# Kernel optimization log

Measured on AMD Instinct MI355X. Metric: run time of the kernel, lower is better.

## Reference

```python
import jax, jax.numpy as jnp
import numpy as np

B, N, H = 2048, 5, 5
IN, HID, OUT = 7, 2048, 512  # IN = 1 + c + c^2 with c = (H-1)//2 = 2


def setup_inputs() -> dict:
    key = jax.random.key(0)
    ks = jax.random.split(key, 7)
    k_in = 1.0 / np.sqrt(IN).astype(np.float32)
    k_h = 1.0 / np.sqrt(HID).astype(np.float32)
    return {
        "ins": jax.random.normal(ks[0], (B, N, H, H), jnp.float32),
        "w1": (jax.random.uniform(ks[1], (4, HID, IN), jnp.float32) - 0.5) * k_in,
        "b1": (jax.random.uniform(ks[2], (HID,), jnp.float32) - 0.5) * k_in,
        "w2": (jax.random.uniform(ks[3], (4, HID, HID), jnp.float32) - 0.5) * k_h,
        "b2": (jax.random.uniform(ks[4], (HID,), jnp.float32) - 0.5) * k_h,
        "w3": (jax.random.uniform(ks[5], (4, OUT, HID), jnp.float32) - 0.5) * k_h,
        "b3": (jax.random.uniform(ks[6], (OUT,), jnp.float32) - 0.5) * k_h,
        "ln_g": jnp.ones((HID,), jnp.float32),
        "ln_b": jnp.zeros((HID,), jnp.float32),
    }


def _rot90(x):
    # matches torch: x.flip(3).permute(0,1,3,2)
    return jnp.swapaxes(jnp.flip(x, axis=3), 2, 3)


def _orbit_stack(x):
    b, n = x.shape[0], x.shape[1]
    c = (x.shape[-1] - 1) // 2  # = 2 for H=5
    center = x[:, :, c, c]  # (B,N)
    parts = []
    xi = x
    for _ in range(4):  # fixed C4 group orbit, not a data loop
        parts.append(xi[:, :, :c, :c + 1].reshape(b, n, -1))  # (B,N,c+c^2)
        xi = _rot90(xi)
    orb = jnp.stack(parts, axis=-1)  # (B,N,c+c^2,4)
    cen = jnp.broadcast_to(center[..., None, None], (b, n, 1, 4))
    out = jnp.concatenate([cen, orb], axis=2)  # (B,N,n_orbits,4)
    return jnp.transpose(out, (0, 1, 3, 2))  # (B,N,4,n_orbits)


def _c4conv(w, bias, x):
    # block-circulant kernel: mat[g,h] = w[(h-g) % 4]
    mat = jnp.stack([jnp.roll(w, i, axis=0) for i in range(4)], axis=0)  # (4,4,out,in)
    return jnp.einsum('ghij,bnhj->bngi', mat, x) + bias


def _layernorm(x, g, b, eps=1e-5):
    m = jnp.mean(x, axis=-1, keepdims=True)
    v = jnp.mean(jnp.square(x - m), axis=-1, keepdims=True)
    return (x - m) / jnp.sqrt(v + eps) * g + b


def reference(ins, w1, b1, w2, b2, w3, b3, ln_g, ln_b):
    h = _orbit_stack(ins)                          # (B,N,4,7)
    h = jax.nn.relu(_c4conv(w1, b1, h))            # (B,N,4,HID)
    h = jax.nn.relu(_layernorm(_c4conv(w2, b2, h), ln_g, ln_b))
    return _c4conv(w3, b3, h)                      # (B,N,4,OUT)
```

## Files before the change

kernel.cpp:

```cpp
#include <hip/hip_runtime.h>
#include <stdint.h>


#define HID 2048
#define MROWS 10240

typedef float floatx4 __attribute__((ext_vector_type(4)));
typedef __bf16 bf16x8 __attribute__((ext_vector_type(8)));

__device__ __forceinline__ unsigned short f2bf(float f) {
  union { float f; unsigned int u; } v; v.f = f;
  unsigned int r = v.u + 0x7fffu + ((v.u >> 16) & 1u);
  return (unsigned short)(r >> 16);
}
__device__ __forceinline__ float bf2f(unsigned short s) {
  union { unsigned int u; float f; } v; v.u = ((unsigned int)s) << 16;
  return v.f;
}

template <int NO>
__global__ __launch_bounds__(256) void wtrans_kernel(const float* __restrict__ w,
                                                     unsigned short* __restrict__ W0s,
                                                     unsigned short* __restrict__ W2s,
                                                     unsigned short* __restrict__ Bc) {
  int idx = blockIdx.x * 256 + threadIdx.x;
  int i = idx >> 9, j4 = idx & 511;
  const float4* wp = (const float4*)w;
  float4 w0 = wp[0 * NO * 512 + i * 512 + j4];
  float4 w1 = wp[1 * NO * 512 + i * 512 + j4];
  float4 w2 = wp[2 * NO * 512 + i * 512 + j4];
  float4 w3 = wp[3 * NO * 512 + i * 512 + j4];
  ushort4 s0, s2, vr, vi, nvi;
#define DO(c)                                        \
  s0.c = f2bf(w0.c + w1.c + w2.c + w3.c);            \
  s2.c = f2bf(w0.c - w1.c + w2.c - w3.c);            \
  vr.c = f2bf(w0.c - w2.c);                          \
  vi.c = f2bf(w1.c - w3.c);                          \
  nvi.c = f2bf(-(w1.c - w3.c));
  DO(x) DO(y) DO(z) DO(w)
#undef DO
  ((ushort4*)W0s)[i * 512 + j4] = s0;
  ((ushort4*)W2s)[i * 512 + j4] = s2;
  ((ushort4*)Bc)[i * 1024 + j4] = vr;
  ((ushort4*)Bc)[i * 1024 + 512 + j4] = nvi;
  ((ushort4*)Bc)[(NO + i) * 1024 + j4] = vi;
  ((ushort4*)Bc)[(NO + i) * 1024 + 512 + j4] = vr;
}

__global__ __launch_bounds__(256) void layer1_kernel(const float* __restrict__ ins,
                                                     const float* __restrict__ w1,
                                                     const float* __restrict__ b1,
                                                     unsigned short* __restrict__ h1s,
                                                     int row0) {
  __shared__ float orbs[32][28];
  int t = threadIdx.x;
  int b0 = blockIdx.x * 32;
  int i = blockIdx.y * 256 + t;
  if (t < 32) {
    const float* x = ins + (size_t)(row0 + b0 + t) * 25;
    float v[25];
#pragma unroll
    for (int p = 0; p < 25; ++p) v[p] = x[p];
    float* o = orbs[t];
    o[0] = v[12]; o[7] = v[12]; o[14] = v[12]; o[21] = v[12];
#pragma unroll
    for (int r = 0; r < 2; ++r)
#pragma unroll
      for (int c = 0; c < 3; ++c) {
        int m = 1 + r * 3 + c;
        o[m]      = v[r * 5 + c];
        o[7 + m]  = v[c * 5 + (4 - r)];
        o[14 + m] = v[(4 - r) * 5 + (4 - c)];
        o[21 + m] = v[(4 - c) * 5 + r];
      }
  }
  __syncthreads();
  float w[4][7];
#pragma unroll
  for (int r = 0; r < 4; ++r)
#pragma unroll
    for (int j = 0; j < 7; ++j) w[r][j] = w1[(r * HID + i) * 7 + j];
  float bias = b1[i];
  for (int s = 0; s < 32; ++s) {
    float a[4] = {bias, bias, bias, bias};
#pragma unroll
    for (int hh = 0; hh < 4; ++hh)
#pragma unroll
      for (int j = 0; j < 7; ++j) {
        float ov = orbs[s][hh * 7 + j];
#pragma unroll
        for (int g = 0; g < 4; ++g) a[g] += w[(hh - g) & 3][j] * ov;
      }
    float h0 = fmaxf(a[0], 0.f), h1 = fmaxf(a[1], 0.f);
    float h2 = fmaxf(a[2], 0.f), h3 = fmaxf(a[3], 0.f);
    size_t base = (size_t)(b0 + s) * 8192 + i;
    h1s[base]        = f2bf(h0 + h1 + h2 + h3);
    h1s[base + 2048] = f2bf(h0 - h1 + h2 - h3);
    h1s[base + 4096] = f2bf(h0 - h2);
    h1s[base + 6144] = f2bf(h3 - h1);
  }
}


__global__ __launch_bounds__(512, 2) void gemm_spec(const unsigned short* __restrict__ A,
                                                    const unsigned short* __restrict__ B0,
                                                    const unsigned short* __restrict__ B1,
                                                    const unsigned short* __restrict__ B2,
                                                    float* __restrict__ Cf,
                                                    unsigned short* __restrict__ Cb,
                                                    int s1, int s2, int N0, int ldc,
                                                    int NT, int NTL, int MTN) {
  __shared__ __align__(16) unsigned short As[2][16384];
  __shared__ __align__(16) unsigned short Bs[2][16384];
  int tid = threadIdx.x;
  int wave = tid >> 6, lane = tid & 63;
  int lane15 = lane & 15, lane4 = lane >> 4, l7 = lane15 & 7;
  int wm = wave >> 2, wn = wave & 3;
  int wm64 = wm << 6, wn32 = wn << 5;

  int srow = tid >> 3;
  int scol = ((tid & 7) ^ ((tid >> 3) & 7)) << 3;
  int bs64 = (srow >> 5) << 6;

#define STA(buf, mh, kk)                                                                              \
  __builtin_amdgcn_global_load_lds(                                                                   \
      (const __attribute__((address_space(1))) void*)(Agb + (size_t)((mh) * 64) * 8192 + (kk)),       \
      (__attribute__((address_space(3))) void*)((char*)As[buf] + (mh) * 16384 + wave * 1024),         \
      16, 0, 0);                                                                                      \
  __builtin_amdgcn_global_load_lds(                                                                   \
      (const __attribute__((address_space(1))) void*)(Agb + (size_t)((mh) * 64 + 128) * 8192 + (kk)), \
      (__attribute__((address_space(3))) void*)((char*)As[buf] + (mh) * 16384 + 8192 + wave * 1024),  \
      16, 0, 0)

#define STB(buf, nh, kk)                                                                              \
  __builtin_amdgcn_global_load_lds(                                                                   \
      (const __attribute__((address_space(1))) void*)(Bgb + (size_t)(bs64 + (nh) * 32) * ldb + (kk)), \
      (__attribute__((address_space(3))) void*)((char*)Bs[buf] + (nh) * 16384 + wave * 1024),         \
      16, 0, 0);                                                                                      \
  __builtin_amdgcn_global_load_lds(                                                                   \
      (const __attribute__((address_space(1))) void*)(Bgb + (size_t)(bs64 + 128 + (nh) * 32) * ldb + (kk)), \
      (__attribute__((address_space(3))) void*)((char*)Bs[buf] + (nh) * 16384 + 8192 + wave * 1024),  \
      16, 0, 0)

#define RAF(buf, mh)                                                                                  \
  _Pragma("unroll") for (int mi_ = 0; mi_ < 4; ++mi_)                                                 \
  _Pragma("unroll") for (int ks_ = 0; ks_ < 2; ++ks_)                                                 \
      af[mi_][ks_] = *(const bf16x8*)((const char*)As[buf] +                                          \
          (((mh) * 128 + wm64 + mi_ * 16 + lane15) << 7) + (((ks_ * 4 + lane4) ^ l7) << 4))

#define RBF(dst, buf, nh)                                                                             \
  _Pragma("unroll") for (int ni_ = 0; ni_ < 2; ++ni_)                                                 \
  _Pragma("unroll") for (int ks_ = 0; ks_ < 2; ++ks_)                                                 \
      dst[ni_][ks_] = *(const bf16x8*)((const char*)Bs[buf] +                                         \
          (((nh) * 128 + wn32 + ni_ * 16 + lane15) << 7) + (((ks_ * 4 + lane4) ^ l7) << 4))

#define MM(mh, nh, bF)                                                                                \
  _Pragma("unroll") for (int mi_ = 0; mi_ < 4; ++mi_)                                                 \
  _Pragma("unroll") for (int ni_ = 0; ni_ < 2; ++ni_)                                                 \
  _Pragma("unroll") for (int ks_ = 0; ks_ < 2; ++ks_)                                                 \
      acc[(mh) * 4 + mi_][(nh) * 2 + ni_] = __builtin_amdgcn_mfma_f32_16x16x32_bf16(                  \
          af[mi_][ks_], bF[ni_][ks_], acc[(mh) * 4 + mi_][(nh) * 2 + ni_], 0, 0, 0)

#define BAR() __builtin_amdgcn_s_barrier()
#define LGKM0() asm volatile("s_waitcnt lgkmcnt(0)" ::: "memory")
#define LGKM8() asm volatile("s_waitcnt lgkmcnt(8)" ::: "memory")
#define VM6() asm volatile("s_waitcnt vmcnt(6)" ::: "memory")

  bf16x8 af[4][2], b0r[2][2], b1r[2][2];
  const floatx4 fz = {0.f, 0.f, 0.f, 0.f};
  floatx4 acc[8][4];

  int G = (int)gridDim.x;
  for (int pass = 0;; ++pass) {
    int base = pass * G;
    if (base >= NT) break;
    int wt = (pass & 1) ? (base + G - 1 - (int)blockIdx.x) : (base + (int)blockIdx.x);
    if (wt >= NT) continue;

    int mt, nt;
    if (wt < NTL) { int j = wt / MTN; nt = s2 + j; mt = wt - j * MTN; }
    else          { int w2_ = wt - NTL; int j = w2_ / MTN; nt = j; mt = w2_ - j * MTN; }
    int m0 = mt * 256;

    const unsigned short* Bp;
    int K, aoff, coff, nloc;
    if (nt < s1)      { Bp = B0; K = 2048; aoff = 0;    coff = 0;      nloc = nt * 256; }
    else if (nt < s2) { Bp = B1; K = 2048; aoff = 2048; coff = N0;     nloc = (nt - s1) * 256; }
    else              { Bp = B2; K = 4096; aoff = 4096; coff = 2 * N0; nloc = (nt - s2) * 256; }
    int ldb = K;

    const unsigned short* Agb = A + (size_t)(m0 + srow) * 8192 + aoff + scol;
    const unsigned short* Bgb = Bp + (size_t)(nloc + (srow & 31)) * ldb + scol;

#pragma unroll
    for (int a = 0; a < 8; ++a)
#pragma unroll
      for (int b = 0; b < 4; ++b) acc[a][b] = fz;

    STA(0, 0, 0); STB(0, 0, 0); STB(0, 1, 0); STA(0, 1, 0);
    STA(1, 0, 64); STB(1, 0, 64); STB(1, 1, 64);
    VM6();
    BAR();

    for (int k0 = 0; k0 < K; k0 += 128) {
      RAF(0, 0); RBF(b0r, 0, 0);
      STA(1, 1, k0 + 64);
      LGKM8();
      BAR(); LGKM0();
      __builtin_amdgcn_s_setprio(1); MM(0, 0, b0r); __builtin_amdgcn_s_setprio(0);
      BAR();
      RBF(b1r, 0, 1);
      STA(0, 0, k0 + 128);
      BAR(); LGKM0();
      __builtin_amdgcn_s_setprio(1); MM(0, 1, b1r); __builtin_amdgcn_s_setprio(0);
      BAR();
      RAF(0, 1);
      STB(0, 0, k0 + 128);
      BAR(); LGKM0();
      __builtin_amdgcn_s_setprio(1); MM(1, 0, b0r); __builtin_amdgcn_s_setprio(0);
      BAR();
      STB(0, 1, k0 + 128);
      BAR(); LGKM0();
      __builtin_amdgcn_s_setprio(1); MM(1, 1, b1r); __builtin_amdgcn_s_setprio(0);
      VM6();
      BAR();
      RAF(1, 0); RBF(b0r, 1, 0);
      STA(0, 1, k0 + 128);
      LGKM8();
      BAR(); LGKM0();
      __builtin_amdgcn_s_setprio(1); MM(0, 0, b0r); __builtin_amdgcn_s_setprio(0);
      BAR();
      RBF(b1r, 1, 1);
      STA(1, 0, k0 + 192);
      BAR(); LGKM0();
      __builtin_amdgcn_s_setprio(1); MM(0, 1, b1r); __builtin_amdgcn_s_setprio(0);
      BAR();
      RAF(1, 1);
      STB(1, 0, k0 + 192);
      BAR(); LGKM0();
      __builtin_amdgcn_s_setprio(1); MM(1, 0, b0r); __builtin_amdgcn_s_setprio(0);
      BAR();
      STB(1, 1, k0 + 192);
      BAR(); LGKM0();
      __builtin_amdgcn_s_setprio(1); MM(1, 1, b1r); __builtin_amdgcn_s_setprio(0);
      VM6();
      BAR();
    }
    asm volatile("s_waitcnt vmcnt(0)" ::: "memory");

#pragma unroll
    for (int ni = 0; ni < 4; ++ni) {
      int col = coff + nloc + wn * 64 + (ni >> 1) * 32 + (ni & 1) * 16 + lane15;
#pragma unroll
      for (int mi = 0; mi < 8; ++mi) {
        int row = m0 + wm * 128 + (mi >> 2) * 64 + (mi & 3) * 16 + lane4 * 4;
        if (Cb) {
#pragma unroll
          for (int r = 0; r < 4; ++r)
            Cb[(size_t)(row + r) * ldc + col] = f2bf(acc[mi][ni][r]);
        } else {
#pragma unroll
          for (int r = 0; r < 4; ++r)
            Cf[(size_t)(row + r) * ldc + col] = acc[mi][ni][r];
        }
      }
    }
  }
#undef STA
#undef STB
#undef RAF
#undef RBF
#undef MM
#undef BAR
#undef LGKM0
#undef LGKM8
#undef VM6
}

__global__ __launch_bounds__(256) void ln_spec_kernel(const unsigned short* C2,
                                                      const float* __restrict__ b2,
                                                      const float* __restrict__ ln_g,
                                                      const float* __restrict__ ln_b,
                                                      unsigned short* h1s) {
  int t = threadIdx.x;
  size_t base = (size_t)blockIdx.x * 8192;
  const ushort4* p = (const ushort4*)(C2 + base);
  const float4* bp2 = (const float4*)b2;
  float4 y[4][2];
  float s[4] = {0, 0, 0, 0}, q[4] = {0, 0, 0, 0};
#pragma unroll
  for (int hl = 0; hl < 2; ++hl) {
    int j = hl * 256 + t;
    ushort4 u0 = p[j], u2 = p[512 + j], ur = p[1024 + j], ui = p[1536 + j];
    float4 bb = bp2[j];
#define DO(c)                                                   \
  {                                                             \
    float v0 = bf2f(u0.c), v2 = bf2f(u2.c);                     \
    float vr = bf2f(ur.c), vi = bf2f(ui.c);                     \
    float e0 = 0.25f * (v0 + v2 + 2.f * vr) + bb.c;             \
    float e1 = 0.25f * (v0 - v2 - 2.f * vi) + bb.c;             \
    float e2 = 0.25f * (v0 + v2 - 2.f * vr) + bb.c;             \
    float e3 = 0.25f * (v0 - v2 + 2.f * vi) + bb.c;             \
    y[0][hl].c = e0; y[1][hl].c = e1; y[2][hl].c = e2; y[3][hl].c = e3; \
    s[0] += e0; q[0] += e0 * e0; s[1] += e1; q[1] += e1 * e1;   \
    s[2] += e2; q[2] += e2 * e2; s[3] += e3; q[3] += e3 * e3;   \
  }
    DO(x) DO(y) DO(z) DO(w)
#undef DO
  }
#pragma unroll
  for (int off = 32; off > 0; off >>= 1)
#pragma unroll
    for (int g = 0; g < 4; ++g) {
      s[g] += __shfl_down(s[g], off, 64);
      q[g] += __shfl_down(q[g], off, 64);
    }
  __shared__ float rs[4][4], rq[4][4];
  int w = t >> 6, l = t & 63;
  if (l == 0)
#pragma unroll
    for (int g = 0; g < 4; ++g) { rs[w][g] = s[g]; rq[w][g] = q[g]; }
  __syncthreads();
  float mean[4], rstd[4];
#pragma unroll
  for (int g = 0; g < 4; ++g) {
    float ss = rs[0][g] + rs[1][g] + rs[2][g] + rs[3][g];
    float qq = rq[0][g] + rq[1][g] + rq[2][g] + rq[3][g];
    mean[g] = ss * (1.f / HID);
    float var = qq * (1.f / HID) - mean[g] * mean[g];
    rstd[g] = rsqrtf(var + 1e-5f);
  }
  const float4* gp = (const float4*)ln_g;
  const float4* lbp = (const float4*)ln_b;
#pragma unroll
  for (int hl = 0; hl < 2; ++hl) {
    int j = hl * 256 + t;
    float4 gg = gp[j], lb = lbp[j];
    ushort4 o[4];
#define DO(c)                                                               \
  {                                                                         \
    float h0 = fmaxf((y[0][hl].c - mean[0]) * rstd[0] * gg.c + lb.c, 0.f);  \
    float h1 = fmaxf((y[1][hl].c - mean[1]) * rstd[1] * gg.c + lb.c, 0.f);  \
    float h2 = fmaxf((y[2][hl].c - mean[2]) * rstd[2] * gg.c + lb.c, 0.f);  \
    float h3 = fmaxf((y[3][hl].c - mean[3]) * rstd[3] * gg.c + lb.c, 0.f);  \
    o[0].c = f2bf(h0 + h1 + h2 + h3);                                       \
    o[1].c = f2bf(h0 - h1 + h2 - h3);                                       \
    o[2].c = f2bf(h0 - h2);                                                 \
    o[3].c = f2bf(h3 - h1);                                                 \
  }
    DO(x) DO(y) DO(z) DO(w)
#undef DO
    size_t ob = (size_t)blockIdx.x * 8192;
#pragma unroll
    for (int pl = 0; pl < 4; ++pl)
      ((ushort4*)(h1s + ob + pl * 2048))[j] = o[pl];
  }
}

__global__ __launch_bounds__(256) void out_ep_kernel(const float* __restrict__ Z,
                                                     const float* __restrict__ b3,
                                                     float* __restrict__ out) {
  int e = blockIdx.x * 256 + threadIdx.x;
  int row = e >> 9, i = e & 511;
  size_t base = (size_t)row * 2048;
  float z0 = Z[base + i], z2 = Z[base + 512 + i];
  float zr = Z[base + 1024 + i], zi = Z[base + 1536 + i];
  float bv = b3[i];
  out[base + i]        = 0.25f * (z0 + z2 + 2.f * zr) + bv;
  out[base + 512 + i]  = 0.25f * (z0 - z2 - 2.f * zi) + bv;
  out[base + 1024 + i] = 0.25f * (z0 + z2 - 2.f * zr) + bv;
  out[base + 1536 + i] = 0.25f * (z0 - z2 + 2.f * zi) + bv;
}

extern "C" void kernel_launch(void* const* d_in, const int* in_sizes, int n_in,
                              void* d_out, int out_size, void* d_ws, size_t ws_size,
                              hipStream_t stream) {
  const float* ins = (const float*)d_in[0];
  const float* w1  = (const float*)d_in[1];
  const float* b1  = (const float*)d_in[2];
  const float* w2  = (const float*)d_in[3];
  const float* b2  = (const float*)d_in[4];
  const float* w3  = (const float*)d_in[5];
  const float* b3  = (const float*)d_in[6];
  const float* lng = (const float*)d_in[7];
  const float* lnb = (const float*)d_in[8];
  float* out = (float*)d_out;
  char* ws = (char*)d_ws;

  unsigned short* W0s2 = (unsigned short*)ws;
  unsigned short* W2s2 = W0s2 + 4194304;
  unsigned short* Bc2  = W2s2 + 4194304;
  unsigned short* W0s3 = Bc2 + 16777216;
  unsigned short* W2s3 = W0s3 + 1048576;
  unsigned short* Bc3  = W2s3 + 1048576;
  const size_t WT_BYTES = 62914560ull;
  char* chunk_base = ws + WT_BYTES;

  wtrans_kernel<2048><<<4096, 256, 0, stream>>>(w2, W0s2, W2s2, Bc2);
  wtrans_kernel<512><<<1024, 256, 0, stream>>>(w3, W0s3, W2s3, Bc3);

  const size_t H1_BYTES = (size_t)5120 * 8192 * 2;
  const size_t H2_BYTES = (size_t)MROWS * 8192 * 2;
  const size_t need_full = WT_BYTES + H1_BYTES + H2_BYTES + 4096;

  if (ws_size >= need_full) {
    unsigned short* h1s = (unsigned short*)chunk_base;
    float*          Z   = (float*)chunk_base;
    unsigned short* H2  = (unsigned short*)(chunk_base + H1_BYTES);
    const int Mc = 5120, MTN = Mc / 256;
    for (int c = 0; c < 2; ++c) {
      int row0 = c * Mc;
      unsigned short* H2c = H2 + (size_t)row0 * 8192;
      layer1_kernel<<<dim3(Mc / 32, 8), 256, 0, stream>>>(ins, w1, b1, h1s, row0);
      gemm_spec<<<256, 512, 0, stream>>>(h1s, W0s2, W2s2, Bc2, nullptr, H2c,
                                         8, 16, 2048, 8192, 32 * MTN, 16 * MTN, MTN);
      ln_spec_kernel<<<Mc, 256, 0, stream>>>(H2c, b2, lng, lnb, H2c);
    }
    {
      const int MT3 = MROWS / 256;
      gemm_spec<<<256, 512, 0, stream>>>(H2, W0s3, W2s3, Bc3, Z, nullptr,
                                         2, 4, 512, 2048, 8 * MT3, 4 * MT3, MT3);
      out_ep_kernel<<<MROWS * 2, 256, 0, stream>>>(Z, b3, out);
    }
  } else {
    static const int Pcand[8] = {1, 2, 4, 5, 8, 10, 20, 40};
    int P = 40;
    for (int pi = 0; pi < 8; ++pi) {
      size_t mc = (size_t)MROWS / Pcand[pi];
      size_t need = WT_BYTES + mc * 8192 * 2 * 2 + 4096;
      if (need <= ws_size) { P = Pcand[pi]; break; }
    }
    const int Mc = MROWS / P, MTN = Mc / 256;
    unsigned short* h1s = (unsigned short*)chunk_base;
    unsigned short* C2  = (unsigned short*)(chunk_base + (size_t)Mc * 8192 * 2);
    float*          Z   = (float*)C2;
    for (int c = 0; c < P; ++c) {
      int row0 = c * Mc;
      layer1_kernel<<<dim3(Mc / 32, 8), 256, 0, stream>>>(ins, w1, b1, h1s, row0);
      gemm_spec<<<256, 512, 0, stream>>>(h1s, W0s2, W2s2, Bc2, nullptr, C2,
                                         8, 16, 2048, 8192, 32 * MTN, 16 * MTN, MTN);
      ln_spec_kernel<<<Mc, 256, 0, stream>>>(C2, b2, lng, lnb, h1s);
      gemm_spec<<<256, 512, 0, stream>>>(h1s, W0s3, W2s3, Bc3, Z, nullptr,
                                         2, 4, 512, 2048, 8 * MTN, 4 * MTN, MTN);
      out_ep_kernel<<<Mc * 2, 256, 0, stream>>>(Z, b3, out + (size_t)row0 * 2048);
    }
  }
}
```

Baseline: 1.001 ms.

## Merge layer-2 chunks into one GEMM using output buffer as scratch, band tile order

```diff
diff --git a/kernel.cpp b/kernel.cpp
--- a/kernel.cpp
+++ b/kernel.cpp
@@ -50,8 +50,9 @@
 __global__ __launch_bounds__(256) void layer1_kernel(const float* __restrict__ ins,
                                                      const float* __restrict__ w1,
                                                      const float* __restrict__ b1,
-                                                     unsigned short* __restrict__ h1s,
-                                                     int row0) {
+                                                     unsigned short* __restrict__ hlo,
+                                                     unsigned short* __restrict__ hhi,
+                                                     int msplit, int row0) {
   __shared__ float orbs[32][28];
   int t = threadIdx.x;
   int b0 = blockIdx.x * 32;
@@ -93,23 +94,28 @@
       }
     float h0 = fmaxf(a[0], 0.f), h1 = fmaxf(a[1], 0.f);
     float h2 = fmaxf(a[2], 0.f), h3 = fmaxf(a[3], 0.f);
-    size_t base = (size_t)(b0 + s) * 8192 + i;
-    h1s[base]        = f2bf(h0 + h1 + h2 + h3);
-    h1s[base + 2048] = f2bf(h0 - h1 + h2 - h3);
-    h1s[base + 4096] = f2bf(h0 - h2);
-    h1s[base + 6144] = f2bf(h3 - h1);
-  }
-}
-
-
-__global__ __launch_bounds__(512, 2) void gemm_spec(const unsigned short* __restrict__ A,
+    int orow = b0 + s;
+    unsigned short* hp = (orow < msplit) ? hlo + (size_t)orow * 8192
+                                         : hhi + (size_t)(orow - msplit) * 8192;
+    hp[i]        = f2bf(h0 + h1 + h2 + h3);
+    hp[2048 + i] = f2bf(h0 - h1 + h2 - h3);
+    hp[4096 + i] = f2bf(h0 - h2);
+    hp[6144 + i] = f2bf(h3 - h1);
+  }
+}
+
+
+__global__ __launch_bounds__(512, 2) void gemm_spec(const unsigned short* __restrict__ Alo,
+                                                    const unsigned short* __restrict__ Ahi,
+                                                    int MS,
                                                     const unsigned short* __restrict__ B0,
                                                     const unsigned short* __restrict__ B1,
                                                     const unsigned short* __restrict__ B2,
                                                     float* __restrict__ Cf,
                                                     unsigned short* __restrict__ Cb,
                                                     int s1, int s2, int N0, int ldc,
-                                                    int NT, int NTL, int MTN) {
+                                                    int NT, int NTL, int MTN,
+                                                    int CL, int CS) {
   __shared__ __align__(16) unsigned short As[2][16384];
   __shared__ __align__(16) unsigned short Bs[2][16384];
   int tid = threadIdx.x;
@@ -121,6 +127,7 @@
   int srow = tid >> 3;
   int scol = ((tid & 7) ^ ((tid >> 3) & 7)) << 3;
   int bs64 = (srow >> 5) << 6;
+  int BH = (MTN % 8 == 0) ? 8 : ((MTN % 4 == 0) ? 4 : 1);
 
 #define STA(buf, mh, kk)                                                                              \
   __builtin_amdgcn_global_load_lds(                                                                   \
@@ -165,6 +172,7 @@
 #define LGKM0() asm volatile("s_waitcnt lgkmcnt(0)" ::: "memory")
 #define LGKM8() asm volatile("s_waitcnt lgkmcnt(8)" ::: "memory")
 #define VM6() asm volatile("s_waitcnt vmcnt(6)" ::: "memory")
+#define VM8() asm volatile("s_waitcnt vmcnt(8)" ::: "memory")
 
   bf16x8 af[4][2], b0r[2][2], b1r[2][2];
   const floatx4 fz = {0.f, 0.f, 0.f, 0.f};
@@ -178,8 +186,16 @@
     if (wt >= NT) continue;
 
     int mt, nt;
-    if (wt < NTL) { int j = wt / MTN; nt = s2 + j; mt = wt - j * MTN; }
-    else          { int w2_ = wt - NTL; int j = w2_ / MTN; nt = j; mt = w2_ - j * MTN; }
+    if (wt < NTL) {
+      int per = CL * BH;
+      int band = wt / per, r = wt % per;
+      nt = s2 + r % CL; mt = band * BH + r / CL;
+    } else {
+      int j = wt - NTL;
+      int per = CS * BH;
+      int band = j / per, r = j % per;
+      nt = r % CS; mt = band * BH + r / CS;
+    }
     int m0 = mt * 256;
 
     const unsigned short* Bp;
@@ -189,7 +205,9 @@
     else              { Bp = B2; K = 4096; aoff = 4096; coff = 2 * N0; nloc = (nt - s2) * 256; }
     int ldb = K;
 
-    const unsigned short* Agb = A + (size_t)(m0 + srow) * 8192 + aoff + scol;
+    const unsigned short* Ab = (m0 < MS) ? (Alo + (size_t)m0 * 8192)
+                                         : (Ahi + (size_t)(m0 - MS) * 8192);
+    const unsigned short* Agb = Ab + (size_t)srow * 8192 + aoff + scol;
     const unsigned short* Bgb = Bp + (size_t)(nloc + (srow & 31)) * ldb + scol;
 
 #pragma unroll
@@ -198,49 +216,51 @@
       for (int b = 0; b < 4; ++b) acc[a][b] = fz;
 
     STA(0, 0, 0); STB(0, 0, 0); STB(0, 1, 0); STA(0, 1, 0);
-    STA(1, 0, 64); STB(1, 0, 64); STB(1, 1, 64);
-    VM6();
+    STA(1, 0, 64); STB(1, 0, 64); STB(1, 1, 64); STA(1, 1, 64);
+    VM8();
     BAR();
 
     for (int k0 = 0; k0 < K; k0 += 128) {
+      int ka = k0 + 128; if (ka >= K) ka = 0;
+      int kb = k0 + 192; if (kb >= K) kb = 0;
       RAF(0, 0); RBF(b0r, 0, 0);
-      STA(1, 1, k0 + 64);
       LGKM8();
       BAR(); LGKM0();
       __builtin_amdgcn_s_setprio(1); MM(0, 0, b0r); __builtin_amdgcn_s_setprio(0);
       BAR();
       RBF(b1r, 0, 1);
-      STA(0, 0, k0 + 128);
+      STA(0, 0, ka);
       BAR(); LGKM0();
       __builtin_amdgcn_s_setprio(1); MM(0, 1, b1r); __builtin_amdgcn_s_setprio(0);
       BAR();
       RAF(0, 1);
-      STB(0, 0, k0 + 128);
+      STB(0, 0, ka);
       BAR(); LGKM0();
       __builtin_amdgcn_s_setprio(1); MM(1, 0, b0r); __builtin_amdgcn_s_setprio(0);
       BAR();
-      STB(0, 1, k0 + 128);
+      STB(0, 1, ka);
       BAR(); LGKM0();
       __builtin_amdgcn_s_setprio(1); MM(1, 1, b1r); __builtin_amdgcn_s_setprio(0);
       VM6();
       BAR();
       RAF(1, 0); RBF(b0r, 1, 0);
-      STA(0, 1, k0 + 128);
+      STA(0, 1, ka);
       LGKM8();
       BAR(); LGKM0();
       __builtin_amdgcn_s_setprio(1); MM(0, 0, b0r); __builtin_amdgcn_s_setprio(0);
       BAR();
       RBF(b1r, 1, 1);
-      STA(1, 0, k0 + 192);
+      STA(1, 0, kb);
       BAR(); LGKM0();
       __builtin_amdgcn_s_setprio(1); MM(0, 1, b1r); __builtin_amdgcn_s_setprio(0);
       BAR();
       RAF(1, 1);
-      STB(1, 0, k0 + 192);
+      STB(1, 0, kb);
       BAR(); LGKM0();
       __builtin_amdgcn_s_setprio(1); MM(1, 0, b0r); __builtin_amdgcn_s_setprio(0);
       BAR();
-      STB(1, 1, k0 + 192);
+      STB(1, 1, kb);
+      STA(1, 1, kb);
       BAR(); LGKM0();
       __builtin_amdgcn_s_setprio(1); MM(1, 1, b1r); __builtin_amdgcn_s_setprio(0);
       VM6();
@@ -275,6 +295,7 @@
 #undef LGKM0
 #undef LGKM8
 #undef VM6
+#undef VM8
 }
 
 __global__ __launch_bounds__(256) void ln_spec_kernel(const unsigned short* C2,
@@ -386,6 +407,7 @@
   const float* lnb = (const float*)d_in[8];
   float* out = (float*)d_out;
   char* ws = (char*)d_ws;
+  const int BIGMS = 0x40000000;
 
   unsigned short* W0s2 = (unsigned short*)ws;
   unsigned short* W2s2 = W0s2 + 4194304;
@@ -399,29 +421,23 @@
   wtrans_kernel<2048><<<4096, 256, 0, stream>>>(w2, W0s2, W2s2, Bc2);
   wtrans_kernel<512><<<1024, 256, 0, stream>>>(w3, W0s3, W2s3, Bc3);
 
-  const size_t H1_BYTES = (size_t)5120 * 8192 * 2;
-  const size_t H2_BYTES = (size_t)MROWS * 8192 * 2;
-  const size_t need_full = WT_BYTES + H1_BYTES + H2_BYTES + 4096;
-
-  if (ws_size >= need_full) {
-    unsigned short* h1s = (unsigned short*)chunk_base;
-    float*          Z   = (float*)chunk_base;
-    unsigned short* H2  = (unsigned short*)(chunk_base + H1_BYTES);
-    const int Mc = 5120, MTN = Mc / 256;
-    for (int c = 0; c < 2; ++c) {
-      int row0 = c * Mc;
-      unsigned short* H2c = H2 + (size_t)row0 * 8192;
-      layer1_kernel<<<dim3(Mc / 32, 8), 256, 0, stream>>>(ins, w1, b1, h1s, row0);
-      gemm_spec<<<256, 512, 0, stream>>>(h1s, W0s2, W2s2, Bc2, nullptr, H2c,
-                                         8, 16, 2048, 8192, 32 * MTN, 16 * MTN, MTN);
-      ln_spec_kernel<<<Mc, 256, 0, stream>>>(H2c, b2, lng, lnb, H2c);
-    }
-    {
-      const int MT3 = MROWS / 256;
-      gemm_spec<<<256, 512, 0, stream>>>(H2, W0s3, W2s3, Bc3, Z, nullptr,
-                                         2, 4, 512, 2048, 8 * MT3, 4 * MT3, MT3);
-      out_ep_kernel<<<MROWS * 2, 256, 0, stream>>>(Z, b3, out);
-    }
+  const size_t H1L_BYTES = (size_t)5120 * 8192 * 2;
+  const size_t H2_BYTES  = (size_t)MROWS * 8192 * 2;
+  const size_t need_merged = WT_BYTES + H1L_BYTES + H2_BYTES + 4096;
+
+  if (ws_size >= need_merged && (size_t)out_size >= (size_t)5120 * 8192 * 2) {
+    unsigned short* h1lo = (unsigned short*)chunk_base;
+    unsigned short* h1hi = (unsigned short*)out;
+    float*          Z    = (float*)chunk_base;
+    unsigned short* H2   = (unsigned short*)(chunk_base + H1L_BYTES);
+    const int MTN = MROWS / 256;
+    layer1_kernel<<<dim3(MROWS / 32, 8), 256, 0, stream>>>(ins, w1, b1, h1lo, h1hi, 5120, 0);
+    gemm_spec<<<256, 512, 0, stream>>>(h1lo, h1hi, 5120, W0s2, W2s2, Bc2, nullptr, H2,
+                                       8, 16, 2048, 8192, 32 * MTN, 16 * MTN, MTN, 16, 16);
+    ln_spec_kernel<<<MROWS, 256, 0, stream>>>(H2, b2, lng, lnb, H2);
+    gemm_spec<<<256, 512, 0, stream>>>(H2, H2, BIGMS, W0s3, W2s3, Bc3, Z, nullptr,
+                                       2, 4, 512, 2048, 8 * MTN, 4 * MTN, MTN, 4, 4);
+    out_ep_kernel<<<MROWS * 2, 256, 0, stream>>>(Z, b3, out);
   } else {
     static const int Pcand[8] = {1, 2, 4, 5, 8, 10, 20, 40};
     int P = 40;
@@ -436,12 +452,12 @@
     float*          Z   = (float*)C2;
     for (int c = 0; c < P; ++c) {
       int row0 = c * Mc;
-      layer1_kernel<<<dim3(Mc / 32, 8), 256, 0, stream>>>(ins, w1, b1, h1s, row0);
-      gemm_spec<<<256, 512, 0, stream>>>(h1s, W0s2, W2s2, Bc2, nullptr, C2,
-                                         8, 16, 2048, 8192, 32 * MTN, 16 * MTN, MTN);
+      layer1_kernel<<<dim3(Mc / 32, 8), 256, 0, stream>>>(ins, w1, b1, h1s, h1s, BIGMS, row0);
+      gemm_spec<<<256, 512, 0, stream>>>(h1s, h1s, BIGMS, W0s2, W2s2, Bc2, nullptr, C2,
+                                         8, 16, 2048, 8192, 32 * MTN, 16 * MTN, MTN, 16, 16);
       ln_spec_kernel<<<Mc, 256, 0, stream>>>(C2, b2, lng, lnb, h1s);
-      gemm_spec<<<256, 512, 0, stream>>>(h1s, W0s3, W2s3, Bc3, Z, nullptr,
-                                         2, 4, 512, 2048, 8 * MTN, 4 * MTN, MTN);
+      gemm_spec<<<256, 512, 0, stream>>>(h1s, h1s, BIGMS, W0s3, W2s3, Bc3, Z, nullptr,
+                                         2, 4, 512, 2048, 8 * MTN, 4 * MTN, MTN, 4, 4);
       out_ep_kernel<<<Mc * 2, 256, 0, stream>>>(Z, b3, out + (size_t)row0 * 2048);
     }
   }
```

Measured after the change: 1.080 ms. 7.8% more time.

## Switch GEMM to 32x32x16 MFMA, reorder prefetch schedule, vectorize output epilogue

Applied to the files above, without the earlier changes.

```diff
diff --git a/kernel.cpp b/kernel.cpp
--- a/kernel.cpp
+++ b/kernel.cpp
@@ -6,6 +6,7 @@
 #define MROWS 10240
 
 typedef float floatx4 __attribute__((ext_vector_type(4)));
+typedef float floatx16 __attribute__((ext_vector_type(16)));
 typedef __bf16 bf16x8 __attribute__((ext_vector_type(8)));
 
 __device__ __forceinline__ unsigned short f2bf(float f) {
@@ -114,7 +115,7 @@
   __shared__ __align__(16) unsigned short Bs[2][16384];
   int tid = threadIdx.x;
   int wave = tid >> 6, lane = tid & 63;
-  int lane15 = lane & 15, lane4 = lane >> 4, l7 = lane15 & 7;
+  int l31 = lane & 31, lane5 = lane >> 5, l7 = lane & 7;
   int wm = wave >> 2, wn = wave & 3;
   int wm64 = wm << 6, wn32 = wn << 5;
 
@@ -143,32 +144,30 @@
       16, 0, 0)
 
 #define RAF(buf, mh)                                                                                  \
-  _Pragma("unroll") for (int mi_ = 0; mi_ < 4; ++mi_)                                                 \
-  _Pragma("unroll") for (int ks_ = 0; ks_ < 2; ++ks_)                                                 \
-      af[mi_][ks_] = *(const bf16x8*)((const char*)As[buf] +                                          \
-          (((mh) * 128 + wm64 + mi_ * 16 + lane15) << 7) + (((ks_ * 4 + lane4) ^ l7) << 4))
+  _Pragma("unroll") for (int rb_ = 0; rb_ < 2; ++rb_)                                                 \
+  _Pragma("unroll") for (int j_ = 0; j_ < 4; ++j_)                                                    \
+      af[rb_][j_] = *(const bf16x8*)((const char*)As[buf] +                                           \
+          (((mh) * 128 + wm64 + rb_ * 32 + l31) << 7) + (((2 * j_ + lane5) ^ l7) << 4))
 
 #define RBF(dst, buf, nh)                                                                             \
-  _Pragma("unroll") for (int ni_ = 0; ni_ < 2; ++ni_)                                                 \
-  _Pragma("unroll") for (int ks_ = 0; ks_ < 2; ++ks_)                                                 \
-      dst[ni_][ks_] = *(const bf16x8*)((const char*)Bs[buf] +                                         \
-          (((nh) * 128 + wn32 + ni_ * 16 + lane15) << 7) + (((ks_ * 4 + lane4) ^ l7) << 4))
+  _Pragma("unroll") for (int j_ = 0; j_ < 4; ++j_)                                                    \
+      dst[j_] = *(const bf16x8*)((const char*)Bs[buf] +                                               \
+          (((nh) * 128 + wn32 + l31) << 7) + (((2 * j_ + lane5) ^ l7) << 4))
 
 #define MM(mh, nh, bF)                                                                                \
-  _Pragma("unroll") for (int mi_ = 0; mi_ < 4; ++mi_)                                                 \
-  _Pragma("unroll") for (int ni_ = 0; ni_ < 2; ++ni_)                                                 \
-  _Pragma("unroll") for (int ks_ = 0; ks_ < 2; ++ks_)                                                 \
-      acc[(mh) * 4 + mi_][(nh) * 2 + ni_] = __builtin_amdgcn_mfma_f32_16x16x32_bf16(                  \
-          af[mi_][ks_], bF[ni_][ks_], acc[(mh) * 4 + mi_][(nh) * 2 + ni_], 0, 0, 0)
+  _Pragma("unroll") for (int j_ = 0; j_ < 4; ++j_)                                                    \
+  _Pragma("unroll") for (int rb_ = 0; rb_ < 2; ++rb_)                                                 \
+      acc[(mh) * 2 + rb_][nh] = __builtin_amdgcn_mfma_f32_32x32x16_bf16(                              \
+          af[rb_][j_], bF[j_], acc[(mh) * 2 + rb_][nh], 0, 0, 0)
 
 #define BAR() __builtin_amdgcn_s_barrier()
 #define LGKM0() asm volatile("s_waitcnt lgkmcnt(0)" ::: "memory")
 #define LGKM8() asm volatile("s_waitcnt lgkmcnt(8)" ::: "memory")
 #define VM6() asm volatile("s_waitcnt vmcnt(6)" ::: "memory")
-
-  bf16x8 af[4][2], b0r[2][2], b1r[2][2];
-  const floatx4 fz = {0.f, 0.f, 0.f, 0.f};
-  floatx4 acc[8][4];
+#define VM8() asm volatile("s_waitcnt vmcnt(8)" ::: "memory")
+
+  bf16x8 af[2][4], b0r[4], b1r[4];
+  floatx16 acc[4][2];
 
   int G = (int)gridDim.x;
   for (int pass = 0;; ++pass) {
@@ -193,54 +192,58 @@
     const unsigned short* Bgb = Bp + (size_t)(nloc + (srow & 31)) * ldb + scol;
 
 #pragma unroll
-    for (int a = 0; a < 8; ++a)
-#pragma unroll
-      for (int b = 0; b < 4; ++b) acc[a][b] = fz;
+    for (int a = 0; a < 4; ++a)
+#pragma unroll
+      for (int b = 0; b < 2; ++b)
+#pragma unroll
+        for (int e = 0; e < 16; ++e) acc[a][b][e] = 0.f;
 
     STA(0, 0, 0); STB(0, 0, 0); STB(0, 1, 0); STA(0, 1, 0);
-    STA(1, 0, 64); STB(1, 0, 64); STB(1, 1, 64);
-    VM6();
+    STA(1, 0, 64); STB(1, 0, 64); STB(1, 1, 64); STA(1, 1, 64);
+    VM8();
     BAR();
 
     for (int k0 = 0; k0 < K; k0 += 128) {
+      int ka = k0 + 128; if (ka >= K) ka = 0;
+      int kb = k0 + 192; if (kb >= K) kb = 0;
       RAF(0, 0); RBF(b0r, 0, 0);
-      STA(1, 1, k0 + 64);
       LGKM8();
       BAR(); LGKM0();
       __builtin_amdgcn_s_setprio(1); MM(0, 0, b0r); __builtin_amdgcn_s_setprio(0);
       BAR();
       RBF(b1r, 0, 1);
-      STA(0, 0, k0 + 128);
+      STA(0, 0, ka);
       BAR(); LGKM0();
       __builtin_amdgcn_s_setprio(1); MM(0, 1, b1r); __builtin_amdgcn_s_setprio(0);
       BAR();
       RAF(0, 1);
-      STB(0, 0, k0 + 128);
+      STB(0, 0, ka);
       BAR(); LGKM0();
       __builtin_amdgcn_s_setprio(1); MM(1, 0, b0r); __builtin_amdgcn_s_setprio(0);
       BAR();
-      STB(0, 1, k0 + 128);
+      STB(0, 1, ka);
       BAR(); LGKM0();
       __builtin_amdgcn_s_setprio(1); MM(1, 1, b1r); __builtin_amdgcn_s_setprio(0);
       VM6();
       BAR();
       RAF(1, 0); RBF(b0r, 1, 0);
-      STA(0, 1, k0 + 128);
+      STA(0, 1, ka);
       LGKM8();
       BAR(); LGKM0();
       __builtin_amdgcn_s_setprio(1); MM(0, 0, b0r); __builtin_amdgcn_s_setprio(0);
       BAR();
       RBF(b1r, 1, 1);
-      STA(1, 0, k0 + 192);
+      STA(1, 0, kb);
       BAR(); LGKM0();
       __builtin_amdgcn_s_setprio(1); MM(0, 1, b1r); __builtin_amdgcn_s_setprio(0);
       BAR();
       RAF(1, 1);
-      STB(1, 0, k0 + 192);
+      STB(1, 0, kb);
       BAR(); LGKM0();
       __builtin_amdgcn_s_setprio(1); MM(1, 0, b0r); __builtin_amdgcn_s_setprio(0);
       BAR();
-      STB(1, 1, k0 + 192);
+      STB(1, 1, kb);
+      STA(1, 1, kb);
       BAR(); LGKM0();
       __builtin_amdgcn_s_setprio(1); MM(1, 1, b1r); __builtin_amdgcn_s_setprio(0);
       VM6();
@@ -249,19 +252,20 @@
     asm volatile("s_waitcnt vmcnt(0)" ::: "memory");
 
 #pragma unroll
-    for (int ni = 0; ni < 4; ++ni) {
-      int col = coff + nloc + wn * 64 + (ni >> 1) * 32 + (ni & 1) * 16 + lane15;
-#pragma unroll
-      for (int mi = 0; mi < 8; ++mi) {
-        int row = m0 + wm * 128 + (mi >> 2) * 64 + (mi & 3) * 16 + lane4 * 4;
-        if (Cb) {
-#pragma unroll
-          for (int r = 0; r < 4; ++r)
-            Cb[(size_t)(row + r) * ldc + col] = f2bf(acc[mi][ni][r]);
-        } else {
-#pragma unroll
-          for (int r = 0; r < 4; ++r)
-            Cf[(size_t)(row + r) * ldc + col] = acc[mi][ni][r];
+    for (int nh = 0; nh < 2; ++nh) {
+      int col = coff + nloc + wn * 64 + nh * 32 + l31;
+#pragma unroll
+      for (int rbi = 0; rbi < 4; ++rbi) {
+        int rowb = m0 + wm * 128 + (rbi >> 1) * 64 + (rbi & 1) * 32 + lane5 * 4;
+#pragma unroll
+        for (int rq = 0; rq < 4; ++rq) {
+#pragma unroll
+          for (int dr = 0; dr < 4; ++dr) {
+            int row = rowb + rq * 8 + dr;
+            float v = acc[rbi][nh][rq * 4 + dr];
+            if (Cb) Cb[(size_t)row * ldc + col] = f2bf(v);
+            else    Cf[(size_t)row * ldc + col] = v;
+          }
         }
       }
     }
@@ -275,6 +279,7 @@
 #undef LGKM0
 #undef LGKM8
 #undef VM6
+#undef VM8
 }
 
 __global__ __launch_bounds__(256) void ln_spec_kernel(const unsigned short* C2,
@@ -361,15 +366,26 @@
                                                      const float* __restrict__ b3,
                                                      float* __restrict__ out) {
   int e = blockIdx.x * 256 + threadIdx.x;
-  int row = e >> 9, i = e & 511;
-  size_t base = (size_t)row * 2048;
-  float z0 = Z[base + i], z2 = Z[base + 512 + i];
-  float zr = Z[base + 1024 + i], zi = Z[base + 1536 + i];
-  float bv = b3[i];
-  out[base + i]        = 0.25f * (z0 + z2 + 2.f * zr) + bv;
-  out[base + 512 + i]  = 0.25f * (z0 - z2 - 2.f * zi) + bv;
-  out[base + 1024 + i] = 0.25f * (z0 + z2 - 2.f * zr) + bv;
-  out[base + 1536 + i] = 0.25f * (z0 - z2 + 2.f * zi) + bv;
+  int row = e >> 7, i4 = e & 127;
+  const float4* Z4 = (const float4*)Z;
+  const float4* b34 = (const float4*)b3;
+  float4* o4 = (float4*)out;
+  size_t base = (size_t)row * 512;
+  float4 z0 = Z4[base + i4],       z2 = Z4[base + 128 + i4];
+  float4 zr = Z4[base + 256 + i4], zi = Z4[base + 384 + i4];
+  float4 bv = b34[i4];
+  float4 e0, e1, e2, e3;
+#define DO(c)                                     \
+  e0.c = 0.25f * (z0.c + z2.c + 2.f * zr.c) + bv.c; \
+  e1.c = 0.25f * (z0.c - z2.c - 2.f * zi.c) + bv.c; \
+  e2.c = 0.25f * (z0.c + z2.c - 2.f * zr.c) + bv.c; \
+  e3.c = 0.25f * (z0.c - z2.c + 2.f * zi.c) + bv.c;
+  DO(x) DO(y) DO(z) DO(w)
+#undef DO
+  o4[base + i4]       = e0;
+  o4[base + 128 + i4] = e1;
+  o4[base + 256 + i4] = e2;
+  o4[base + 384 + i4] = e3;
 }
 
 extern "C" void kernel_launch(void* const* d_in, const int* in_sizes, int n_in,
@@ -420,7 +436,7 @@
       const int MT3 = MROWS / 256;
       gemm_spec<<<256, 512, 0, stream>>>(H2, W0s3, W2s3, Bc3, Z, nullptr,
                                          2, 4, 512, 2048, 8 * MT3, 4 * MT3, MT3);
-      out_ep_kernel<<<MROWS * 2, 256, 0, stream>>>(Z, b3, out);
+      out_ep_kernel<<<MROWS / 2, 256, 0, stream>>>(Z, b3, out);
     }
   } else {
     static const int Pcand[8] = {1, 2, 4, 5, 8, 10, 20, 40};
@@ -442,7 +458,7 @@
       ln_spec_kernel<<<Mc, 256, 0, stream>>>(C2, b2, lng, lnb, h1s);
       gemm_spec<<<256, 512, 0, stream>>>(h1s, W0s3, W2s3, Bc3, Z, nullptr,
                                          2, 4, 512, 2048, 8 * MTN, 4 * MTN, MTN);
-      out_ep_kernel<<<Mc * 2, 256, 0, stream>>>(Z, b3, out + (size_t)row0 * 2048);
-    }
-  }
-}
+      out_ep_kernel<<<Mc / 2, 256, 0, stream>>>(Z, b3, out + (size_t)row0 * 2048);
+    }
+  }
+}
```

After: 1.019 ms. Within noise of the previous version (+1.7%).
